# Kernel optimization log

Measured on AMD Instinct MI355X. Metric: run time of the kernel, lower is better.

The kernel has to match this reference:

```python
import jax, jax.numpy as jnp
import numpy as np

B, S, D = 1, 2048, 2048
HQ, HKV = 32, 8
HD = D // HQ          # 64
G = HQ // HKV         # 4 query heads per kv head


def apply_rope(x, freq):
    # x: (b, h, s, hd); freq: (s, hd//2) angles. Llama-style pairwise rotation.
    cos = jnp.cos(freq)  # (s, hd//2)
    sin = jnp.sin(freq)
    xr = x.reshape(*x.shape[:-1], HD // 2, 2)
    xe, xo = xr[..., 0], xr[..., 1]
    re = xe * cos - xo * sin
    ro = xe * sin + xo * cos
    return jnp.stack([re, ro], axis=-1).reshape(x.shape)


def setup_inputs() -> dict:
    key = jax.random.key(0)
    k1, k2, k3, k4, k5 = jax.random.split(key, 5)
    x = jax.random.normal(k1, (B, S, D), dtype=jnp.float32)
    # RoPE angles: pos * inv_freq, theta=10000
    inv_freq = 1.0 / (10000.0 ** (jnp.arange(0, HD, 2, dtype=jnp.float32) / HD))
    freq = jnp.arange(S, dtype=jnp.float32)[:, None] * inv_freq[None, :]  # (S, HD//2)
    mask = jnp.tril(jnp.ones((S, S), dtype=jnp.int32))
    scale = D ** -0.5
    wq = jax.random.normal(k2, (D, HQ * HD), dtype=jnp.float32) * scale
    wk = jax.random.normal(k3, (D, HKV * HD), dtype=jnp.float32) * scale
    wv = jax.random.normal(k4, (D, HKV * HD), dtype=jnp.float32) * scale
    wo = jax.random.normal(k5, (HQ * HD, D), dtype=jnp.float32) * scale
    return {"x": x, "freq": freq, "mask": mask, "wq": wq, "wk": wk, "wv": wv, "wo": wo}


def reference(x, freq, mask, wq, wk, wv, wo):
    b, s, d = x.shape
    q = (x @ wq).reshape(b, s, HQ, HD).transpose(0, 2, 1, 3)    # (b,HQ,s,hd)
    k = (x @ wk).reshape(b, s, HKV, HD).transpose(0, 2, 1, 3)   # (b,HKV,s,hd)
    v = (x @ wv).reshape(b, s, HKV, HD).transpose(0, 2, 1, 3)
    q = apply_rope(q, freq[:s])
    k = apply_rope(k, freq[:s])
    # GQA: broadcast kv heads over groups instead of repeat_interleave
    qg = q.reshape(b, HKV, G, s, HD)
    scores = jnp.einsum('bhgsd,bhtd->bhgst', qg, k)             # (b,HKV,G,s,s)
    scores = jnp.where(mask[:s, :s] == 0, -jnp.inf, scores)
    w = jax.nn.softmax(scores * (HD ** -0.5), axis=-1)
    out = jnp.einsum('bhgst,bhtd->bhgsd', w, v)
    out = out.reshape(b, HQ, s, HD).transpose(0, 2, 1, 3).reshape(b, s, HQ * HD)
    return out @ wo
```

## Files before the change

### kernel.cpp

```cpp
#include <hip/hip_runtime.h>

typedef unsigned short u16;
typedef unsigned int u32;
typedef unsigned long long u64;

using bf16x8 = __bf16 __attribute__((ext_vector_type(8)));
using f32x4  = float  __attribute__((ext_vector_type(4)));

#define LDS_SPACE __attribute__((address_space(3)))
#define GLB_SPACE __attribute__((address_space(1)))

static __device__ __forceinline__ u16 f2bf(float f) {
  union { float f; u32 u; } c; c.f = f;
  u32 u = c.u;
  return (u16)((u + 0x7fffu + ((u >> 16) & 1u)) >> 16);
}
static __device__ __forceinline__ float bf2f(u16 u) {
  union { u32 u; float f; } c; c.u = ((u32)u) << 16;
  return c.f;
}

static __device__ __forceinline__ void fence_barrier() {
  asm volatile("" ::: "memory");
  __builtin_amdgcn_s_barrier();
  asm volatile("" ::: "memory");
}

constexpr float SC = 0.18033688011112042f;

__global__ __launch_bounds__(256) void prep_k(const float* __restrict__ x,
                                              const float* __restrict__ wq,
                                              const float* __restrict__ wk,
                                              const float* __restrict__ wv,
                                              const float* __restrict__ wo,
                                              u16* __restrict__ x_bf,
                                              u16* __restrict__ wqkv_t,
                                              u16* __restrict__ wo_t) {
  const int b = blockIdx.x;
  if (b < 4096) {
    int i = b * 256 + threadIdx.x;
    float4 v = ((const float4*)x)[i];
    ushort4 o;
    o.x = f2bf(v.x); o.y = f2bf(v.y); o.z = f2bf(v.z); o.w = f2bf(v.w);
    ((ushort4*)x_bf)[i] = o;
    return;
  }
  const float* src; u16* dst; int C, bx, by; float scale = 1.0f;
  if (b < 8192)      { src = wq; dst = wqkv_t; C = 2048; int t = b - 4096; bx = t & 63; by = t >> 6; scale = SC; }
  else if (b < 9216) { src = wk; dst = wqkv_t + (size_t)2048 * 2048; C = 512; int t = b - 8192; bx = t & 15; by = t >> 4; }
  else if (b < 10240){ src = wv; dst = wqkv_t + (size_t)2560 * 2048; C = 512; int t = b - 9216; bx = t & 15; by = t >> 4; }
  else               { src = wo; dst = wo_t; C = 2048; int t = b - 10240; bx = t & 63; by = t >> 6; }
  __shared__ float t[32][33];
  const int lx = threadIdx.x & 31, ly = threadIdx.x >> 5;
  const int r0 = by * 32, c0 = bx * 32;
  #pragma unroll
  for (int i = 0; i < 32; i += 8)
    t[ly + i][lx] = src[(size_t)(r0 + ly + i) * C + c0 + lx];
  __syncthreads();
  #pragma unroll
  for (int i = 0; i < 32; i += 8)
    dst[(size_t)(c0 + ly + i) * 2048 + r0 + lx] = f2bf(t[lx][ly + i] * scale);
}

__global__ __launch_bounds__(256) void vtrans_k(const u16* __restrict__ Y,
                                                u16* __restrict__ Vt) {
  __shared__ u16 t[64][72];
  const int s0 = blockIdx.x * 64;
  const int c0 = blockIdx.y * 64;
  const int lx = threadIdx.x & 63, ly = threadIdx.x >> 6;
  #pragma unroll
  for (int i = 0; i < 64; i += 4)
    t[i + ly][lx] = Y[(size_t)(s0 + i + ly) * 3072 + 2560 + c0 + lx];
  __syncthreads();
  #pragma unroll
  for (int i = 0; i < 64; i += 4)
    Vt[(size_t)(c0 + i + ly) * 2048 + s0 + lx] = t[lx][i + ly];
}

template <typename OutT, int BN>
__global__ __launch_bounds__(256) void gemm64_k(const u16* __restrict__ A,
                                                const u16* __restrict__ Bt,
                                                OutT* __restrict__ C,
                                                int M, int N, int K) {
  constexpr int WN = BN / 32;
  __shared__ u16 As[2][64 * 64];
  __shared__ u16 Bs[2][BN * 64];
  const int tid = threadIdx.x, lane = tid & 63, w = tid >> 6;
  const int wr = w >> 1, wc = w & 1;
  const int bm = blockIdx.y, bn = blockIdx.x;
  const int l15 = lane & 15, lq = lane >> 4;
  f32x4 acc[2][WN] = {};

  const int srow8 = lane >> 3;
  const int scolb = ((lane & 7) ^ srow8) * 16;
  const u16* AgR = A + (size_t)(bm * 64 + w * 16 + srow8) * K;
  const u16* BgR = Bt + (size_t)(bn * BN + w * (BN / 4) + srow8) * K;

  auto stage = [&](int buf, int k0) {
    #pragma unroll
    for (int i = 0; i < 2; ++i)
      __builtin_amdgcn_global_load_lds(
          (const GLB_SPACE u32*)((const char*)(AgR + (size_t)i * 8 * K + k0) + scolb),
          (LDS_SPACE u32*)&As[buf][(w * 16 + i * 8) * 64], 16, 0, 0);
    #pragma unroll
    for (int i = 0; i < WN; ++i)
      __builtin_amdgcn_global_load_lds(
          (const GLB_SPACE u32*)((const char*)(BgR + (size_t)i * 8 * K + k0) + scolb),
          (LDS_SPACE u32*)&Bs[buf][(w * (BN / 4) + i * 8) * 64], 16, 0, 0);
  };

  stage(0, 0);
  asm volatile("s_waitcnt vmcnt(0)" ::: "memory");
  fence_barrier();

  for (int k0 = 0; k0 < K; k0 += 64) {
    const int p = (k0 >> 6) & 1;
    if (k0 + 64 < K) stage(p ^ 1, k0 + 64);

    #pragma unroll
    for (int kk = 0; kk < 2; ++kk) {
      bf16x8 a[2], b[WN];
      #pragma unroll
      for (int m = 0; m < 2; ++m) {
        const int ra = wr * 32 + m * 16 + l15;
        a[m] = *(const bf16x8*)&As[p][ra * 64 + (((kk * 4 + lq) ^ (ra & 7)) << 3)];
      }
      #pragma unroll
      for (int n = 0; n < WN; ++n) {
        const int rb = wc * (BN / 2) + n * 16 + l15;
        b[n] = *(const bf16x8*)&Bs[p][rb * 64 + (((kk * 4 + lq) ^ (rb & 7)) << 3)];
      }
      #pragma unroll
      for (int m = 0; m < 2; ++m)
        #pragma unroll
        for (int n = 0; n < WN; ++n)
          acc[m][n] = __builtin_amdgcn_mfma_f32_16x16x32_bf16(a[m], b[n], acc[m][n], 0, 0, 0);
    }

    asm volatile("s_waitcnt vmcnt(0)" ::: "memory");
    fence_barrier();
  }

  const int r0 = bm * 64 + wr * 32 + lq * 4;
  const int c0 = bn * BN + wc * (BN / 2) + l15;
  #pragma unroll
  for (int m = 0; m < 2; ++m)
    #pragma unroll
    for (int n = 0; n < WN; ++n)
      #pragma unroll
      for (int r = 0; r < 4; ++r) {
        float v = acc[m][n][r];
        size_t off = (size_t)(r0 + m * 16 + r) * N + (c0 + n * 16);
        if constexpr (sizeof(OutT) == 2) ((u16*)C)[off] = f2bf(v);
        else C[off] = v;
      }
}

__global__ __launch_bounds__(256) void rope_k(u16* __restrict__ Y,
                                              const float* __restrict__ freq) {
  int idx = blockIdx.x * 256 + threadIdx.x;
  int s = idx / 1280;
  int rem = idx - s * 1280;
  int h = rem >> 5;
  int i = rem & 31;
  int col = (h < 32) ? (h * 64 + 2 * i) : (2048 + (h - 32) * 64 + 2 * i);
  float ang = freq[s * 32 + i];
  float sn, cs;
  sincosf(ang, &sn, &cs);
  size_t base = (size_t)s * 3072 + col;
  float e = bf2f(Y[base]), o = bf2f(Y[base + 1]);
  Y[base]     = f2bf(e * cs - o * sn);
  Y[base + 1] = f2bf(e * sn + o * cs);
}

__global__ __launch_bounds__(256, 3) void attn_part_k(const u16* __restrict__ Y,
                                                      const u16* __restrict__ Vtg,
                                                      u16* __restrict__ Opart,
                                                      float2* __restrict__ Ml,
                                                      u16* __restrict__ Out) {
  __shared__ u16 Ks[2][64 * 64];
  __shared__ u16 Vs[2][64 * 64];
  __shared__ u32 Ps[4][16 * 32];
  const int w = threadIdx.x >> 6, lane = threadIdx.x & 63;
  const int l15 = lane & 15, lq = lane >> 4;

  const int b = (int)blockIdx.x;
  const int head = b & 31;
  const int idx = b >> 5;
  const u64 tb = (idx < 12) ? 986161012810415591ULL : 1200400570313029ULL;
  const int v = (int)((tb >> ((idx < 12 ? idx : idx - 12) * 5)) & 31);
  const int qt = v & 15, ch = v >> 4;
  const int kvh = head >> 2;
  const int ntiles = 2 * qt + 2;
  const int half = qt + 1;
  const int tstart = ch ? half : 0;
  const int tend = (qt >= 8 && ch == 0) ? half : ntiles;
  const int q0w = qt * 128 + w * 32;

  const int srow = lane >> 3;
  const int scolb = ((lane & 7) ^ srow) * 16;
  const char* gkB = (const char*)(Y + (size_t)(w * 16 + srow) * 3072 + 2048 + kvh * 64) + scolb;
  const char* gvB = (const char*)(Vtg + (size_t)(kvh * 64 + w * 16 + srow) * 2048) + scolb;

  auto stage = [&](int buf, int t) {
    const size_t t0 = (size_t)t * 64;
    #pragma unroll
    for (int i = 0; i < 2; ++i) {
      __builtin_amdgcn_global_load_lds((const GLB_SPACE u32*)(gkB + t0 * 6144 + (size_t)i * 49152),
                                       (LDS_SPACE u32*)&Ks[buf][(w * 16 + i * 8) * 64], 16, 0, 0);
      __builtin_amdgcn_global_load_lds((const GLB_SPACE u32*)(gvB + t0 * 2 + (size_t)i * 32768),
                                       (LDS_SPACE u32*)&Vs[buf][(w * 16 + i * 8) * 64], 16, 0, 0);
    }
  };

  int rowB[4], xk[2], pwr[4], prd[2];
  #pragma unroll
  for (int kt = 0; kt < 4; ++kt) rowB[kt] = (kt * 16 + l15) * 128;
  #pragma unroll
  for (int kk = 0; kk < 2; ++kk) xk[kk] = (((kk * 4 + lq) ^ (l15 & 7)) << 4);
  #pragma unroll
  for (int n = 0; n < 4; ++n)
    pwr[n] = (l15 * 32 + ((lq * 2 + n * 8) ^ ((l15 & 7) << 2))) * 4;
  #pragma unroll
  for (int c = 0; c < 2; ++c)
    prd[c] = l15 * 128 + (((c * 32 + lq * 8) ^ ((l15 & 7) << 3)) << 1);

  bf16x8 qf[2][2];
  #pragma unroll
  for (int qs = 0; qs < 2; ++qs)
    #pragma unroll
    for (int kk = 0; kk < 2; ++kk)
      qf[qs][kk] = *(const bf16x8*)&Y[(size_t)(q0w + qs * 16 + l15) * 3072 +
                                      head * 64 + kk * 32 + lq * 8];

  float m_[2] = { -1e30f, -1e30f };
  float l_[2] = { 0.f, 0.f };
  f32x4 accO[2][4] = {};

  stage(0, tstart);
  asm volatile("s_waitcnt vmcnt(0)" ::: "memory");
  fence_barrier();

  for (int t = tstart; t < tend; ++t) {
    const int p = (t - tstart) & 1;
    stage(p ^ 1, (t + 1 < tend) ? t + 1 : t);

    const int t0 = t * 64;
    if (t0 <= q0w + 31) {
      const char* KbC = (const char*)Ks[p];
      const char* VbC = (const char*)Vs[p];

      f32x4 sc[2][4] = {};
      #pragma unroll
      for (int kk = 0; kk < 2; ++kk)
        #pragma unroll
        for (int kt = 0; kt < 4; ++kt) {
          bf16x8 a = *(const bf16x8*)(KbC + rowB[kt] + xk[kk]);
          sc[0][kt] = __builtin_amdgcn_mfma_f32_16x16x32_bf16(a, qf[0][kk], sc[0][kt], 0, 0, 0);
          sc[1][kt] = __builtin_amdgcn_mfma_f32_16x16x32_bf16(a, qf[1][kk], sc[1][kt], 0, 0, 0);
        }

      bf16x8 vf[2][4];
      #pragma unroll
      for (int c = 0; c < 2; ++c)
        #pragma unroll
        for (int dt = 0; dt < 4; ++dt)
          vf[c][dt] = *(const bf16x8*)(VbC + rowB[dt] + xk[c]);

      #pragma unroll
      for (int qs = 0; qs < 2; ++qs) {
        const int qsmin = q0w + qs * 16;
        if (t0 > qsmin + 15) continue;
        const int qrow = qsmin + l15;
        if (t0 + 63 > qsmin) {
          #pragma unroll
          for (int n = 0; n < 4; ++n)
            #pragma unroll
            for (int rr = 0; rr < 4; ++rr)
              if (t0 + n * 16 + lq * 4 + rr > qrow) sc[qs][n][rr] = -1e30f;
        }
        float a0 = fmaxf(fmaxf(sc[qs][0][0], sc[qs][0][1]), fmaxf(sc[qs][0][2], sc[qs][0][3]));
        float a1 = fmaxf(fmaxf(sc[qs][1][0], sc[qs][1][1]), fmaxf(sc[qs][1][2], sc[qs][1][3]));
        float a2 = fmaxf(fmaxf(sc[qs][2][0], sc[qs][2][1]), fmaxf(sc[qs][2][2], sc[qs][2][3]));
        float a3 = fmaxf(fmaxf(sc[qs][3][0], sc[qs][3][1]), fmaxf(sc[qs][3][2], sc[qs][3][3]));
        float mx = fmaxf(fmaxf(a0, a1), fmaxf(a2, a3));

        if (__any(mx > m_[qs] + 7.25f)) {
          float mf = mx;
          mf = fmaxf(mf, __shfl_xor(mf, 16));
          mf = fmaxf(mf, __shfl_xor(mf, 32));
          const float mnew = fmaxf(m_[qs], mf);
          const float alpha = exp2f(m_[qs] - mnew);
          l_[qs] *= alpha;
          #pragma unroll
          for (int dt = 0; dt < 4; ++dt) accO[qs][dt] *= alpha;
          m_[qs] = mnew;
        }
        const float mS = m_[qs];
        float s0 = 0.f, s1 = 0.f, s2 = 0.f, s3 = 0.f;
        char* psB = (char*)Ps[w];
        #pragma unroll
        for (int n = 0; n < 4; ++n) {
          float p0 = exp2f(sc[qs][n][0] - mS);
          float p1 = exp2f(sc[qs][n][1] - mS);
          float p2 = exp2f(sc[qs][n][2] - mS);
          float p3 = exp2f(sc[qs][n][3] - mS);
          s0 += p0; s1 += p1; s2 += p2; s3 += p3;
          u32 w0, w1;
          asm("v_cvt_pk_bf16_f32 %0, %1, %2" : "=v"(w0) : "v"(p0), "v"(p1));
          asm("v_cvt_pk_bf16_f32 %0, %1, %2" : "=v"(w1) : "v"(p2), "v"(p3));
          *(u64*)(psB + pwr[n]) = (u64)w0 | ((u64)w1 << 32);
        }
        l_[qs] += (s0 + s1) + (s2 + s3);

        #pragma unroll
        for (int c = 0; c < 2; ++c) {
          bf16x8 bb = *(const bf16x8*)(psB + prd[c]);
          #pragma unroll
          for (int dt = 0; dt < 4; ++dt)
            accO[qs][dt] = __builtin_amdgcn_mfma_f32_16x16x32_bf16(vf[c][dt], bb, accO[qs][dt], 0, 0, 0);
        }
      }
    }

    asm volatile("s_waitcnt vmcnt(0)" ::: "memory");
    fence_barrier();
  }

  if (qt < 8) {
    #pragma unroll
    for (int qs = 0; qs < 2; ++qs) {
      float lt = l_[qs];
      lt += __shfl_xor(lt, 16);
      lt += __shfl_xor(lt, 32);
      const float rl = 1.0f / lt;
      const int qrow = q0w + qs * 16 + l15;
      #pragma unroll
      for (int dt = 0; dt < 4; ++dt) {
        ushort4 o;
        o.x = f2bf(accO[qs][dt][0] * rl);
        o.y = f2bf(accO[qs][dt][1] * rl);
        o.z = f2bf(accO[qs][dt][2] * rl);
        o.w = f2bf(accO[qs][dt][3] * rl);
        *(ushort4*)&Out[(size_t)qrow * 2048 + head * 64 + dt * 16 + lq * 4] = o;
      }
    }
    return;
  }

  const int slot = ((head << 3) + (qt - 8)) * 2 + ch;
  u16* ob = Opart + (size_t)slot * 8192;
  #pragma unroll
  for (int qs = 0; qs < 2; ++qs) {
    float lt = l_[qs];
    lt += __shfl_xor(lt, 16);
    lt += __shfl_xor(lt, 32);
    const int row = w * 32 + qs * 16 + l15;
    #pragma unroll
    for (int dt = 0; dt < 4; ++dt) {
      ushort4 o;
      o.x = f2bf(accO[qs][dt][0]);
      o.y = f2bf(accO[qs][dt][1]);
      o.z = f2bf(accO[qs][dt][2]);
      o.w = f2bf(accO[qs][dt][3]);
      *(ushort4*)&ob[row * 64 + dt * 16 + lq * 4] = o;
    }
    if (lq == 0) Ml[(size_t)slot * 128 + row] = make_float2(m_[qs], lt);
  }
}

__global__ __launch_bounds__(256) void attn_comb_k(const u16* __restrict__ Opart,
                                                   const float2* __restrict__ Ml,
                                                   u16* __restrict__ Out) {
  const int b = blockIdx.x;
  const int rg = b & 3;
  const int hq = b >> 2;
  const int head = hq >> 3;
  const int qt8 = hq & 7;
  const int slot0 = ((head << 3) + qt8) * 2;
  const int rl = threadIdx.x >> 3;
  const int d8 = (threadIdx.x & 7) * 8;
  const int row = rg * 32 + rl;

  float2 ml0 = Ml[(size_t)slot0 * 128 + row];
  float2 ml1 = Ml[(size_t)(slot0 + 1) * 128 + row];
  const float gm = fmaxf(ml0.x, ml1.x);
  const float a0 = exp2f(ml0.x - gm);
  const float a1 = exp2f(ml1.x - gm);
  const float rd = 1.0f / (a0 * ml0.y + a1 * ml1.y);

  const u16* p0 = &Opart[(size_t)slot0 * 8192 + row * 64 + d8];
  const u16* p1 = &Opart[(size_t)(slot0 + 1) * 8192 + row * 64 + d8];
  ushort4 q0 = *(const ushort4*)p0, q1 = *(const ushort4*)(p0 + 4);
  ushort4 r0 = *(const ushort4*)p1, r1 = *(const ushort4*)(p1 + 4);
  ushort4 o0, o1;
  o0.x = f2bf((a0 * bf2f(q0.x) + a1 * bf2f(r0.x)) * rd);
  o0.y = f2bf((a0 * bf2f(q0.y) + a1 * bf2f(r0.y)) * rd);
  o0.z = f2bf((a0 * bf2f(q0.z) + a1 * bf2f(r0.z)) * rd);
  o0.w = f2bf((a0 * bf2f(q0.w) + a1 * bf2f(r0.w)) * rd);
  o1.x = f2bf((a0 * bf2f(q1.x) + a1 * bf2f(r1.x)) * rd);
  o1.y = f2bf((a0 * bf2f(q1.y) + a1 * bf2f(r1.y)) * rd);
  o1.z = f2bf((a0 * bf2f(q1.z) + a1 * bf2f(r1.z)) * rd);
  o1.w = f2bf((a0 * bf2f(q1.w) + a1 * bf2f(r1.w)) * rd);
  u16* op = &Out[(size_t)((qt8 + 8) * 128 + row) * 2048 + head * 64 + d8];
  *(ushort4*)op = o0;
  *(ushort4*)(op + 4) = o1;
}

extern "C" void kernel_launch(void* const* d_in, const int* in_sizes, int n_in,
                              void* d_out, int out_size, void* d_ws, size_t ws_size,
                              hipStream_t stream) {
  const float* x    = (const float*)d_in[0];
  const float* freq = (const float*)d_in[1];
  const float* wq   = (const float*)d_in[3];
  const float* wk   = (const float*)d_in[4];
  const float* wv   = (const float*)d_in[5];
  const float* wo   = (const float*)d_in[6];
  float* out = (float*)d_out;

  u16* x_bf   = (u16*)d_ws;
  u16* wqkv_t = x_bf + (size_t)2048 * 2048;
  u16* wo_t   = wqkv_t + (size_t)3072 * 2048;
  u16* y      = wo_t + (size_t)2048 * 2048;
  u16* attn   = y + (size_t)2048 * 3072;
  u16* vt     = x_bf;
  u16* opart  = attn + (size_t)2048 * 2048;
  float2* ml  = (float2*)(opart + (size_t)512 * 8192);

  prep_k<<<14336, 256, 0, stream>>>(x, wq, wk, wv, wo, x_bf, wqkv_t, wo_t);
  gemm64_k<u16, 128><<<dim3(24, 32), 256, 0, stream>>>(x_bf, wqkv_t, y, 2048, 3072, 2048);
  rope_k<<<10240, 256, 0, stream>>>(y, freq);
  vtrans_k<<<dim3(32, 8), 256, 0, stream>>>(y, vt);
  attn_part_k<<<768, 256, 0, stream>>>(y, vt, opart, ml, attn);
  attn_comb_k<<<1024, 256, 0, stream>>>(opart, ml, attn);
  gemm64_k<float, 64><<<dim3(32, 32), 256, 0, stream>>>(attn, wo_t, out, 2048, 2048, 2048);
}
```

Measured before the change: 135.8 us.

## Split causal attention KV range into up to four chunks per query tile

```diff
diff --git a/kernel.cpp b/kernel.cpp
--- a/kernel.cpp
+++ b/kernel.cpp
@@ -27,6 +27,15 @@
 }
 
 constexpr float SC = 0.18033688011112042f;
+
+__device__ __constant__ unsigned char kItems[40] = {
+  12, 28, 29, 42, 44, 45, 46, 57, 59, 60, 61, 62, 63,
+  24, 25, 37, 38, 40, 41, 49, 51, 52, 53, 54, 55, 56, 58,
+  8, 20, 21, 32, 33, 34, 36, 48, 50,
+  16, 17,
+  4,
+  0
+};
 
 __global__ __launch_bounds__(256) void prep_k(const float* __restrict__ x,
                                               const float* __restrict__ wq,
@@ -187,14 +196,13 @@
   const int b = (int)blockIdx.x;
   const int head = b & 31;
   const int idx = b >> 5;
-  const u64 tb = (idx < 12) ? 986161012810415591ULL : 1200400570313029ULL;
-  const int v = (int)((tb >> ((idx < 12 ? idx : idx - 12) * 5)) & 31);
-  const int qt = v & 15, ch = v >> 4;
+  const int v = kItems[idx];
+  const int qt = v >> 2, ch = v & 3;
   const int kvh = head >> 2;
   const int ntiles = 2 * qt + 2;
-  const int half = qt + 1;
-  const int tstart = ch ? half : 0;
-  const int tend = (qt >= 8 && ch == 0) ? half : ntiles;
+  const int nch = qt < 4 ? 1 : qt < 8 ? 2 : qt < 12 ? 3 : 4;
+  const int tstart = (ch * ntiles) / nch;
+  const int tend = ((ch + 1) * ntiles) / nch;
   const int q0w = qt * 128 + w * 32;
 
   const int srow = lane >> 3;
@@ -327,7 +335,7 @@
     fence_barrier();
   }
 
-  if (qt < 8) {
+  if (nch == 1) {
     #pragma unroll
     for (int qs = 0; qs < 2; ++qs) {
       float lt = l_[qs];
@@ -348,7 +356,8 @@
     return;
   }
 
-  const int slot = ((head << 3) + (qt - 8)) * 2 + ch;
+  const int off = qt < 8 ? (qt - 4) * 2 : qt < 12 ? 8 + (qt - 8) * 3 : 20 + (qt - 12) * 4;
+  const int slot = head * 36 + off + ch;
   u16* ob = Opart + (size_t)slot * 8192;
   #pragma unroll
   for (int qs = 0; qs < 2; ++qs) {
@@ -375,34 +384,41 @@
   const int b = blockIdx.x;
   const int rg = b & 3;
   const int hq = b >> 2;
-  const int head = hq >> 3;
-  const int qt8 = hq & 7;
-  const int slot0 = ((head << 3) + qt8) * 2;
+  const int head = hq / 12;
+  const int qt = (hq - head * 12) + 4;
+  const int nch = qt < 8 ? 2 : qt < 12 ? 3 : 4;
+  const int off = qt < 8 ? (qt - 4) * 2 : qt < 12 ? 8 + (qt - 8) * 3 : 20 + (qt - 12) * 4;
+  const int slot0 = head * 36 + off;
   const int rl = threadIdx.x >> 3;
   const int d8 = (threadIdx.x & 7) * 8;
   const int row = rg * 32 + rl;
 
-  float2 ml0 = Ml[(size_t)slot0 * 128 + row];
-  float2 ml1 = Ml[(size_t)(slot0 + 1) * 128 + row];
-  const float gm = fmaxf(ml0.x, ml1.x);
-  const float a0 = exp2f(ml0.x - gm);
-  const float a1 = exp2f(ml1.x - gm);
-  const float rd = 1.0f / (a0 * ml0.y + a1 * ml1.y);
-
-  const u16* p0 = &Opart[(size_t)slot0 * 8192 + row * 64 + d8];
-  const u16* p1 = &Opart[(size_t)(slot0 + 1) * 8192 + row * 64 + d8];
-  ushort4 q0 = *(const ushort4*)p0, q1 = *(const ushort4*)(p0 + 4);
-  ushort4 r0 = *(const ushort4*)p1, r1 = *(const ushort4*)(p1 + 4);
+  float gm = -1e30f;
+  #pragma unroll 4
+  for (int c = 0; c < nch; ++c)
+    gm = fmaxf(gm, Ml[(size_t)(slot0 + c) * 128 + row].x);
+  float den = 0.f;
+  float num[8] = {};
+  #pragma unroll 4
+  for (int c = 0; c < nch; ++c) {
+    float2 ml = Ml[(size_t)(slot0 + c) * 128 + row];
+    float a = exp2f(ml.x - gm);
+    den += a * ml.y;
+    const u16* p = &Opart[(size_t)(slot0 + c) * 8192 + row * 64 + d8];
+    ushort4 p0 = *(const ushort4*)p;
+    ushort4 p1 = *(const ushort4*)(p + 4);
+    num[0] += a * bf2f(p0.x); num[1] += a * bf2f(p0.y);
+    num[2] += a * bf2f(p0.z); num[3] += a * bf2f(p0.w);
+    num[4] += a * bf2f(p1.x); num[5] += a * bf2f(p1.y);
+    num[6] += a * bf2f(p1.z); num[7] += a * bf2f(p1.w);
+  }
+  const float rd = 1.0f / den;
   ushort4 o0, o1;
-  o0.x = f2bf((a0 * bf2f(q0.x) + a1 * bf2f(r0.x)) * rd);
-  o0.y = f2bf((a0 * bf2f(q0.y) + a1 * bf2f(r0.y)) * rd);
-  o0.z = f2bf((a0 * bf2f(q0.z) + a1 * bf2f(r0.z)) * rd);
-  o0.w = f2bf((a0 * bf2f(q0.w) + a1 * bf2f(r0.w)) * rd);
-  o1.x = f2bf((a0 * bf2f(q1.x) + a1 * bf2f(r1.x)) * rd);
-  o1.y = f2bf((a0 * bf2f(q1.y) + a1 * bf2f(r1.y)) * rd);
-  o1.z = f2bf((a0 * bf2f(q1.z) + a1 * bf2f(r1.z)) * rd);
-  o1.w = f2bf((a0 * bf2f(q1.w) + a1 * bf2f(r1.w)) * rd);
-  u16* op = &Out[(size_t)((qt8 + 8) * 128 + row) * 2048 + head * 64 + d8];
+  o0.x = f2bf(num[0] * rd); o0.y = f2bf(num[1] * rd);
+  o0.z = f2bf(num[2] * rd); o0.w = f2bf(num[3] * rd);
+  o1.x = f2bf(num[4] * rd); o1.y = f2bf(num[5] * rd);
+  o1.z = f2bf(num[6] * rd); o1.w = f2bf(num[7] * rd);
+  u16* op = &Out[(size_t)(qt * 128 + row) * 2048 + head * 64 + d8];
   *(ushort4*)op = o0;
   *(ushort4*)(op + 4) = o1;
 }
@@ -425,13 +441,13 @@
   u16* attn   = y + (size_t)2048 * 3072;
   u16* vt     = x_bf;
   u16* opart  = attn + (size_t)2048 * 2048;
-  float2* ml  = (float2*)(opart + (size_t)512 * 8192);
+  float2* ml  = (float2*)(opart + (size_t)1152 * 8192);
 
   prep_k<<<14336, 256, 0, stream>>>(x, wq, wk, wv, wo, x_bf, wqkv_t, wo_t);
   gemm64_k<u16, 128><<<dim3(24, 32), 256, 0, stream>>>(x_bf, wqkv_t, y, 2048, 3072, 2048);
   rope_k<<<10240, 256, 0, stream>>>(y, freq);
   vtrans_k<<<dim3(32, 8), 256, 0, stream>>>(y, vt);
-  attn_part_k<<<768, 256, 0, stream>>>(y, vt, opart, ml, attn);
-  attn_comb_k<<<1024, 256, 0, stream>>>(opart, ml, attn);
+  attn_part_k<<<1280, 256, 0, stream>>>(y, vt, opart, ml, attn);
+  attn_comb_k<<<1536, 256, 0, stream>>>(opart, ml, attn);
   gemm64_k<float, 64><<<dim3(32, 32), 256, 0, stream>>>(attn, wo_t, out, 2048, 2048, 2048);
 }
```

Result: no change. 136.7 us (+0.6%).
